# Optimization experiments

Hardware: AMD Instinct MI355X
Metric: run time of the kernel (lower is better)

The kernel has to match this reference:

```python
import jax, jax.numpy as jnp
import numpy as np


def setup_inputs() -> dict:
    key = jax.random.key(0)
    ks = jax.random.split(key, 5)
    B, S, D, E, H = 8, 4096, 512, 4, 64
    x = jax.random.normal(ks[0], (B, S, D), dtype=jnp.float32)
    router_w = jax.random.normal(ks[1], (D, E), dtype=jnp.float32) * 0.02
    router_b = jnp.zeros((E,), dtype=jnp.float32)
    w1 = jax.random.normal(ks[2], (E, D, H), dtype=jnp.float32) * 0.02
    b1 = jnp.zeros((E, H), dtype=jnp.float32)
    w2 = jax.random.normal(ks[3], (E, H, D), dtype=jnp.float32) * 0.02
    b2 = jnp.zeros((E, D), dtype=jnp.float32)
    return {"x": x, "router_w": router_w, "router_b": router_b,
            "w1": w1, "b1": b1, "w2": w2, "b2": b2}


def reference(x, router_w, router_b, w1, b1, w2, b2):
    # Router: softmax over experts. weights: [B, S, E]
    weights = jax.nn.softmax(jnp.einsum('bsd,de->bse', x, router_w) + router_b, axis=-1)
    # All experts run densely on every token (batched over the E axis).
    # h: [B, S, E, H]; TF Dense(activation='gelu') uses exact (non-tanh) gelu.
    h = jax.nn.gelu(jnp.einsum('bsd,edh->bseh', x, w1) + b1, approximate=False)
    # expert outputs: [B, S, E, D]; Dropout is identity at inference.
    expert_out = jnp.einsum('bseh,ehd->bsed', h, w2) + b2
    # weighted sum over experts -> [B, S, D]
    return jnp.sum(expert_out * weights[..., None], axis=2)
```

## Files before the change

### kernel.cpp

```cpp
#include <hip/hip_runtime.h>
#include <hip/hip_bf16.h>
#include <math.h>


typedef short v8s __attribute__((ext_vector_type(8)));
typedef float v4f __attribute__((ext_vector_type(4)));

#define XS 520
#define HS 296
#define TT 32

__device__ __forceinline__ unsigned short f2bf(float f) {
    unsigned int u = __builtin_bit_cast(unsigned int, f);
    u += 0x7fffu + ((u >> 16) & 1u);
    return (unsigned short)(u >> 16);
}

__global__ void moe_prep(const float* __restrict__ w1,
                         const float* __restrict__ w2,
                         const float* __restrict__ b2,
                         const float* __restrict__ rw,
                         unsigned short* __restrict__ w1p,
                         unsigned short* __restrict__ w2p,
                         unsigned short* __restrict__ rp) {
    int idx = blockIdx.x * 256 + threadIdx.x;
    if (idx < 131072) {
        int block = idx >> 9, within = idx & 511;
        int kb = block >> 4, cb = block & 15;
        int n = within >> 5, kl = within & 31;
        int k = kb * 32 + kl;
        int col = cb * 16 + n;
        int e = col >> 6, h = col & 63;
        w1p[idx] = f2bf(w1[(e * 512 + k) * 64 + h]);
    } else if (idx < 131072 + 147456) {
        int op = idx - 131072;
        int block = op >> 9, within = op & 511;
        int kb = block >> 5, cb = block & 31;
        int n = within >> 5, kl = within & 31;
        int k = kb * 32 + kl;
        int d = cb * 16 + n;
        float v = 0.f;
        if (k < 256) {
            int e = k >> 6, h = k & 63;
            v = w2[(e * 64 + h) * 512 + d];
        } else if (k < 260) {
            v = b2[(k - 256) * 512 + d];
        }
        w2p[op] = f2bf(v);
    } else if (idx < 131072 + 147456 + 8192) {
        int op = idx - (131072 + 147456);
        int kb = op >> 9, within = op & 511;
        int n = within >> 5, kl = within & 31;
        int k = kb * 32 + kl;
        float v = (n < 4) ? rw[k * 4 + n] : 0.f;
        rp[op] = f2bf(v);
    }
}

__global__ __launch_bounds__(256, 4)
void moe_main(const float* __restrict__ x,
              const float* __restrict__ rb,
              const float* __restrict__ b1,
              const unsigned short* __restrict__ w1p,
              const unsigned short* __restrict__ w2p,
              const unsigned short* __restrict__ rp,
              float* __restrict__ out) {
    __shared__ __align__(16) unsigned short lx[TT * XS];
    __shared__ float llog[TT * 4];
    __shared__ float lw[TT * 4];

    const int tid  = threadIdx.x;
    const int lane = tid & 63, wv = tid >> 6;
    const int lr = lane & 15, lq = lane >> 4;
    const long t0 = (long)blockIdx.x * TT;

    const float4* xt = (const float4*)(x + t0 * 512);
    #pragma unroll
    for (int it = 0; it < 16; ++it) {
        int F = it * 256 + tid;
        int row = F >> 7, c4 = F & 127;
        float4 v = xt[F];
        unsigned int p0 = (unsigned int)f2bf(v.x) | ((unsigned int)f2bf(v.y) << 16);
        unsigned int p1 = (unsigned int)f2bf(v.z) | ((unsigned int)f2bf(v.w) << 16);
        *(uint2*)&lx[row * XS + c4 * 4] = make_uint2(p0, p1);
    }
    __syncthreads();

    if (wv < 2) {
        v4f accR; accR[0] = accR[1] = accR[2] = accR[3] = 0.f;
        #pragma unroll
        for (int kb = 0; kb < 16; ++kb) {
            v8s a = *(const v8s*)(const void*)&lx[(16 * wv + lr) * XS + kb * 32 + lq * 8];
            v8s b = *(const v8s*)(const void*)&rp[kb * 512 + lr * 32 + lq * 8];
            accR = __builtin_amdgcn_mfma_f32_16x16x32_bf16(a, b, accR, 0, 0, 0);
        }
        if (lr < 4) {
            #pragma unroll
            for (int r = 0; r < 4; ++r)
                llog[(16 * wv + lq * 4 + r) * 4 + lr] = accR[r];
        }
        asm volatile("s_waitcnt lgkmcnt(0)" ::: "memory");
        if (lane < 16) {
            int t = 16 * wv + lane;
            float l[4];
            #pragma unroll
            for (int e = 0; e < 4; ++e) l[e] = llog[t * 4 + e] + rb[e];
            float mx = fmaxf(fmaxf(l[0], l[1]), fmaxf(l[2], l[3]));
            float ex[4], s = 0.f;
            #pragma unroll
            for (int e = 0; e < 4; ++e) { ex[e] = expf(l[e] - mx); s += ex[e]; }
            float inv = 1.f / s;
            #pragma unroll
            for (int e = 0; e < 4; ++e) lw[t * 4 + e] = ex[e] * inv;
        }
    }
    __syncthreads();

    v4f acc1[2][4];
    #pragma unroll
    for (int mt = 0; mt < 2; ++mt)
        #pragma unroll
        for (int nt = 0; nt < 4; ++nt)
            acc1[mt][nt][0] = acc1[mt][nt][1] = acc1[mt][nt][2] = acc1[mt][nt][3] = 0.f;

    for (int kb = 0; kb < 16; ++kb) {
        v8s a[2], b[4];
        #pragma unroll
        for (int mt = 0; mt < 2; ++mt)
            a[mt] = *(const v8s*)(const void*)&lx[(16 * mt + lr) * XS + kb * 32 + lq * 8];
        #pragma unroll
        for (int nt = 0; nt < 4; ++nt)
            b[nt] = *(const v8s*)(const void*)&w1p[(size_t)(kb * 16 + wv * 4 + nt) * 512 + lr * 32 + lq * 8];
        #pragma unroll
        for (int mt = 0; mt < 2; ++mt)
            #pragma unroll
            for (int nt = 0; nt < 4; ++nt)
                acc1[mt][nt] = __builtin_amdgcn_mfma_f32_16x16x32_bf16(a[mt], b[nt], acc1[mt][nt], 0, 0, 0);
    }
    __syncthreads();

    {
        float b1v[4];
        #pragma unroll
        for (int nt = 0; nt < 4; ++nt) b1v[nt] = b1[wv * 64 + nt * 16 + lr];
        #pragma unroll
        for (int mt = 0; mt < 2; ++mt) {
            #pragma unroll
            for (int r = 0; r < 4; ++r) {
                int row = 16 * mt + lq * 4 + r;
                float wt = lw[row * 4 + wv];
                #pragma unroll
                for (int nt = 0; nt < 4; ++nt) {
                    float v = acc1[mt][nt][r] + b1v[nt];
                    float g = 0.5f * v * (1.f + erff(v * 0.70710678118f)) * wt;
                    lx[row * HS + wv * 64 + nt * 16 + lr] = f2bf(g);
                }
            }
        }
        if (tid < 128) {
            int r = tid >> 2, e = tid & 3;
            lx[r * HS + 256 + e] = f2bf(lw[tid]);
            #pragma unroll
            for (int i = 0; i < 7; ++i)
                lx[r * HS + 260 + e + 4 * i] = 0;
        }
    }
    __syncthreads();

    float* ot = out + t0 * 512;
    for (int np = 0; np < 2; ++np) {
        v4f acc2[2][4];
        #pragma unroll
        for (int mt = 0; mt < 2; ++mt)
            #pragma unroll
            for (int nt = 0; nt < 4; ++nt)
                acc2[mt][nt][0] = acc2[mt][nt][1] = acc2[mt][nt][2] = acc2[mt][nt][3] = 0.f;

        for (int kb = 0; kb < 9; ++kb) {
            v8s a[2], b[4];
            #pragma unroll
            for (int mt = 0; mt < 2; ++mt)
                a[mt] = *(const v8s*)(const void*)&lx[(16 * mt + lr) * HS + kb * 32 + lq * 8];
            #pragma unroll
            for (int nt = 0; nt < 4; ++nt)
                b[nt] = *(const v8s*)(const void*)&w2p[(size_t)(kb * 32 + wv * 8 + np * 4 + nt) * 512 + lr * 32 + lq * 8];
            #pragma unroll
            for (int mt = 0; mt < 2; ++mt)
                #pragma unroll
                for (int nt = 0; nt < 4; ++nt)
                    acc2[mt][nt] = __builtin_amdgcn_mfma_f32_16x16x32_bf16(a[mt], b[nt], acc2[mt][nt], 0, 0, 0);
        }

        #pragma unroll
        for (int mt = 0; mt < 2; ++mt)
            #pragma unroll
            for (int nt = 0; nt < 4; ++nt)
                #pragma unroll
                for (int r = 0; r < 4; ++r) {
                    int row = 16 * mt + lq * 4 + r;
                    int col = 128 * wv + 64 * np + 16 * nt + lr;
                    ot[row * 512 + col] = acc2[mt][nt][r];
                }
    }
}

extern "C" void kernel_launch(void* const* d_in, const int* in_sizes, int n_in,
                              void* d_out, int out_size, void* d_ws, size_t ws_size,
                              hipStream_t stream) {
    const float* x  = (const float*)d_in[0];
    const float* rw = (const float*)d_in[1];
    const float* rb = (const float*)d_in[2];
    const float* w1 = (const float*)d_in[3];
    const float* b1 = (const float*)d_in[4];
    const float* w2 = (const float*)d_in[5];
    const float* b2 = (const float*)d_in[6];

    unsigned short* w1p = (unsigned short*)d_ws;
    unsigned short* w2p = w1p + 131072;
    unsigned short* rp  = w2p + 147456;

    moe_prep<<<1120, 256, 0, stream>>>(w1, w2, b2, rw, w1p, w2p, rp);
    moe_main<<<1024, 256, 0, stream>>>(x, rb, b1, w1p, w2p, rp, (float*)d_out);
}
```

Measured before the change: 158.3 us.

## Load x fragments directly from global into MFMA operands, dropping LDS staging

The x tile is no longer staged through LDS as bf16. Each wave reads its A-fragments straight from global memory, converting fp32 to bf16 in registers, for both the router GEMM and the first expert GEMM. This frees LDS (only the h buffer remains) and removes a barrier, so the launch bound is raised to 5 blocks per SM for occupancy. In exchange, every wave re-reads the same x rows from global or cache (four waves times the data), with extra conversion work, and the loads are strided rather than coalesced.

```diff
diff --git a/kernel.cpp b/kernel.cpp
--- a/kernel.cpp
+++ b/kernel.cpp
@@ -6,7 +6,6 @@
 typedef short v8s __attribute__((ext_vector_type(8)));
 typedef float v4f __attribute__((ext_vector_type(4)));
 
-#define XS 520
 #define HS 296
 #define TT 32
 
@@ -14,6 +13,15 @@
     unsigned int u = __builtin_bit_cast(unsigned int, f);
     u += 0x7fffu + ((u >> 16) & 1u);
     return (unsigned short)(u >> 16);
+}
+
+__device__ __forceinline__ v8s cvt8(float4 a, float4 b) {
+    v8s r;
+    r[0] = (short)f2bf(a.x); r[1] = (short)f2bf(a.y);
+    r[2] = (short)f2bf(a.z); r[3] = (short)f2bf(a.w);
+    r[4] = (short)f2bf(b.x); r[5] = (short)f2bf(b.y);
+    r[6] = (short)f2bf(b.z); r[7] = (short)f2bf(b.w);
+    return r;
 }
 
 __global__ void moe_prep(const float* __restrict__ w1,
@@ -57,7 +65,7 @@
     }
 }
 
-__global__ __launch_bounds__(256, 4)
+__global__ __launch_bounds__(256, 5)
 void moe_main(const float* __restrict__ x,
               const float* __restrict__ rb,
               const float* __restrict__ b1,
@@ -65,7 +73,7 @@
               const unsigned short* __restrict__ w2p,
               const unsigned short* __restrict__ rp,
               float* __restrict__ out) {
-    __shared__ __align__(16) unsigned short lx[TT * XS];
+    __shared__ __align__(16) unsigned short lh[TT * HS];
     __shared__ float llog[TT * 4];
     __shared__ float lw[TT * 4];
 
@@ -74,23 +82,14 @@
     const int lr = lane & 15, lq = lane >> 4;
     const long t0 = (long)blockIdx.x * TT;
 
-    const float4* xt = (const float4*)(x + t0 * 512);
-    #pragma unroll
-    for (int it = 0; it < 16; ++it) {
-        int F = it * 256 + tid;
-        int row = F >> 7, c4 = F & 127;
-        float4 v = xt[F];
-        unsigned int p0 = (unsigned int)f2bf(v.x) | ((unsigned int)f2bf(v.y) << 16);
-        unsigned int p1 = (unsigned int)f2bf(v.z) | ((unsigned int)f2bf(v.w) << 16);
-        *(uint2*)&lx[row * XS + c4 * 4] = make_uint2(p0, p1);
-    }
-    __syncthreads();
-
     if (wv < 2) {
+        const float* xr = x + (t0 + 16 * wv + lr) * 512 + lq * 8;
         v4f accR; accR[0] = accR[1] = accR[2] = accR[3] = 0.f;
-        #pragma unroll
+        #pragma unroll 4
         for (int kb = 0; kb < 16; ++kb) {
-            v8s a = *(const v8s*)(const void*)&lx[(16 * wv + lr) * XS + kb * 32 + lq * 8];
+            float4 f0 = *(const float4*)(xr + kb * 32);
+            float4 f1 = *(const float4*)(xr + kb * 32 + 4);
+            v8s a = cvt8(f0, f1);
             v8s b = *(const v8s*)(const void*)&rp[kb * 512 + lr * 32 + lq * 8];
             accR = __builtin_amdgcn_mfma_f32_16x16x32_bf16(a, b, accR, 0, 0, 0);
         }
@@ -114,7 +113,6 @@
             for (int e = 0; e < 4; ++e) lw[t * 4 + e] = ex[e] * inv;
         }
     }
-    __syncthreads();
 
     v4f acc1[2][4];
     #pragma unroll
@@ -123,19 +121,27 @@
         for (int nt = 0; nt < 4; ++nt)
             acc1[mt][nt][0] = acc1[mt][nt][1] = acc1[mt][nt][2] = acc1[mt][nt][3] = 0.f;
 
-    for (int kb = 0; kb < 16; ++kb) {
-        v8s a[2], b[4];
-        #pragma unroll
-        for (int mt = 0; mt < 2; ++mt)
-            a[mt] = *(const v8s*)(const void*)&lx[(16 * mt + lr) * XS + kb * 32 + lq * 8];
-        #pragma unroll
-        for (int nt = 0; nt < 4; ++nt)
-            b[nt] = *(const v8s*)(const void*)&w1p[(size_t)(kb * 16 + wv * 4 + nt) * 512 + lr * 32 + lq * 8];
-        #pragma unroll
-        for (int mt = 0; mt < 2; ++mt)
-            #pragma unroll
-            for (int nt = 0; nt < 4; ++nt)
-                acc1[mt][nt] = __builtin_amdgcn_mfma_f32_16x16x32_bf16(a[mt], b[nt], acc1[mt][nt], 0, 0, 0);
+    {
+        const float* xr0 = x + (t0 + lr) * 512 + lq * 8;
+        const float* xr1 = xr0 + 16 * 512;
+        #pragma unroll 2
+        for (int kb = 0; kb < 16; ++kb) {
+            float4 f00 = *(const float4*)(xr0 + kb * 32);
+            float4 f01 = *(const float4*)(xr0 + kb * 32 + 4);
+            float4 f10 = *(const float4*)(xr1 + kb * 32);
+            float4 f11 = *(const float4*)(xr1 + kb * 32 + 4);
+            v8s a0 = cvt8(f00, f01);
+            v8s a1 = cvt8(f10, f11);
+            v8s b[4];
+            #pragma unroll
+            for (int nt = 0; nt < 4; ++nt)
+                b[nt] = *(const v8s*)(const void*)&w1p[(size_t)(kb * 16 + wv * 4 + nt) * 512 + lr * 32 + lq * 8];
+            #pragma unroll
+            for (int nt = 0; nt < 4; ++nt) {
+                acc1[0][nt] = __builtin_amdgcn_mfma_f32_16x16x32_bf16(a0, b[nt], acc1[0][nt], 0, 0, 0);
+                acc1[1][nt] = __builtin_amdgcn_mfma_f32_16x16x32_bf16(a1, b[nt], acc1[1][nt], 0, 0, 0);
+            }
+        }
     }
     __syncthreads();
 
@@ -153,16 +159,16 @@
                 for (int nt = 0; nt < 4; ++nt) {
                     float v = acc1[mt][nt][r] + b1v[nt];
                     float g = 0.5f * v * (1.f + erff(v * 0.70710678118f)) * wt;
-                    lx[row * HS + wv * 64 + nt * 16 + lr] = f2bf(g);
+                    lh[row * HS + wv * 64 + nt * 16 + lr] = f2bf(g);
                 }
             }
         }
         if (tid < 128) {
             int r = tid >> 2, e = tid & 3;
-            lx[r * HS + 256 + e] = f2bf(lw[tid]);
+            lh[r * HS + 256 + e] = f2bf(lw[tid]);
             #pragma unroll
             for (int i = 0; i < 7; ++i)
-                lx[r * HS + 260 + e + 4 * i] = 0;
+                lh[r * HS + 260 + e + 4 * i] = 0;
         }
     }
     __syncthreads();
@@ -180,7 +186,7 @@
             v8s a[2], b[4];
             #pragma unroll
             for (int mt = 0; mt < 2; ++mt)
-                a[mt] = *(const v8s*)(const void*)&lx[(16 * mt + lr) * HS + kb * 32 + lq * 8];
+                a[mt] = *(const v8s*)(const void*)&lh[(16 * mt + lr) * HS + kb * 32 + lq * 8];
             #pragma unroll
             for (int nt = 0; nt < 4; ++nt)
                 b[nt] = *(const v8s*)(const void*)&w2p[(size_t)(kb * 32 + wv * 8 + np * 4 + nt) * 512 + lr * 32 + lq * 8];
```

After: 180.4 us. 14.0% more time.
